# Kernel tuning notes

Hardware: AMD Instinct MI355X
Metric: run time of the kernel (lower is better)

The kernel has to match this reference:

```python
import jax, jax.numpy as jnp
import numpy as np

V, E = 50000, 800000
NODE_IN, EDGE_IN, OUT, HEADS = 128, 16, 32, 4
NEG_SLOPE = 0.2  # DGL EdgeGATConv default negative_slope


def setup_inputs() -> dict:
    key = jax.random.key(0)
    ks = jax.random.split(key, 10)
    return {
        "node_feats": jax.random.normal(ks[0], (V, NODE_IN), jnp.float32),
        "edge_feats": jax.random.normal(ks[1], (E, EDGE_IN), jnp.float32),
        "src": jax.random.randint(ks[2], (E,), 0, V),
        "dst": jax.random.randint(ks[3], (E,), 0, V),
        "W_node": jax.random.normal(ks[4], (NODE_IN, HEADS * OUT), jnp.float32) * 0.05,
        "W_edge": jax.random.normal(ks[5], (EDGE_IN, HEADS * OUT), jnp.float32) * 0.05,
        "attn_l": jax.random.normal(ks[6], (HEADS, OUT), jnp.float32) * 0.05,
        "attn_r": jax.random.normal(ks[7], (HEADS, OUT), jnp.float32) * 0.05,
        "attn_e": jax.random.normal(ks[8], (HEADS, OUT), jnp.float32) * 0.05,
        "res_W": jax.random.normal(ks[9], (NODE_IN, HEADS * OUT), jnp.float32) * 0.05,
        "bias": jnp.zeros((HEADS * OUT,), jnp.float32),
    }


def _leaky_relu(x, slope):
    return jnp.where(x >= 0, x, slope * x)


def reference(node_feats, edge_feats, src, dst, W_node, W_edge, attn_l, attn_r, attn_e, res_W, bias):
    V = node_feats.shape[0]
    H, F = attn_l.shape
    # linear projections
    ft = (node_feats @ W_node).reshape(V, H, F)    # [V,H,F]
    fe = (edge_feats @ W_edge).reshape(-1, H, F)   # [E,H,F]
    # per-head attention logits
    el = jnp.einsum('vhf,hf->vh', ft, attn_l)      # [V,H]
    er = jnp.einsum('vhf,hf->vh', ft, attn_r)      # [V,H]
    ee = jnp.einsum('ehf,hf->eh', fe, attn_e)      # [E,H]
    e = _leaky_relu(el[src] + er[dst] + ee, NEG_SLOPE)  # [E,H]
    # edge softmax over incoming edges of each destination node (stable)
    emax = jax.ops.segment_max(e, dst, num_segments=V)  # [V,H]
    ex = jnp.exp(e - emax[dst])
    esum = jax.ops.segment_sum(ex, dst, num_segments=V)  # [V,H]
    a = ex / esum[dst]                                   # [E,H]
    # weighted message passing: u_mul_e(ft, a) then sum to dst
    msg = ft[src] * a[:, :, None]                        # [E,H,F]
    rst = jax.ops.segment_sum(msg, dst, num_segments=V)  # [V,H,F]
    # residual connection + bias (EdgeGATConv residual=True, bias=True)
    rst = rst + (node_feats @ res_W).reshape(V, H, F)
    rst = rst + bias.reshape(1, H, F)
    # agg_mode='flatten': concat heads
    return rst.reshape(V, H * F)
```

## Files before the change

kernel.cpp:

```cpp
#include <hip/hip_runtime.h>
#include <hip/hip_fp16.h>
#include <cstdint>

#define V_N 50000
#define E_N 800000
#define NODE_IN 128
#define EDGE_IN 16
#define HF 128
#define NEG_SLOPE 0.2f
#define NBUCKET 782
#define NPART 1563
#define PSZ 512
#define CAP 2048
#define LCAP 1536
#define NODE_BLKS 1563
#define PREP_BLKS 64

#define OFF_FT    0
#define OFF_EL    3200000
#define OFF_ER    3400000
#define OFF_H     3600000
#define OFF_BSUM  4822272
#define OFF_WATT  4823056
#define OFF_BFRAG 4823120
#define OFF_RECB  4839504

typedef short bf16x8 __attribute__((ext_vector_type(8)));
typedef float f32x4 __attribute__((ext_vector_type(4)));

__device__ __forceinline__ unsigned short f2bf(float f) {
    unsigned u = __float_as_uint(f);
    u += 0x7fffu + ((u >> 16) & 1u);
    return (unsigned short)(u >> 16);
}
__device__ __forceinline__ unsigned pk2(float lo, float hi) {
    return (unsigned)f2bf(lo) | ((unsigned)f2bf(hi) << 16);
}
__device__ __forceinline__ float bflo(unsigned w) { return __uint_as_float(w << 16); }
__device__ __forceinline__ float bfhi(unsigned w) { return __uint_as_float(w & 0xffff0000u); }

typedef __fp16 fp16x2 __attribute__((ext_vector_type(2)));
__device__ __forceinline__ unsigned pkh2(float a, float b) {
    fp16x2 h = __builtin_amdgcn_cvt_pkrtz(a, b);
    return __builtin_bit_cast(unsigned, h);
}
__device__ __forceinline__ __half2 u2h(unsigned u) {
    return __builtin_bit_cast(__half2, u);
}
__device__ __forceinline__ unsigned h2u(__half2 h) {
    return __builtin_bit_cast(unsigned, h);
}

__global__ __launch_bounds__(256) void k_prephist(
    const float* __restrict__ We, const float* __restrict__ attn_e,
    const float* __restrict__ Wn, const float* __restrict__ Wr,
    const int* __restrict__ dst,
    float* __restrict__ watt, unsigned* __restrict__ bfrag,
    int* __restrict__ H)
{
    const int t = threadIdx.x;
    if (blockIdx.x >= PREP_BLKS) {
        int hb = blockIdx.x - PREP_BLKS;
        __shared__ int h[NBUCKET];
        for (int i = t; i < NBUCKET; i += 256) h[i] = 0;
        __syncthreads();
        #pragma unroll
        for (int c = 0; c < 2; c++) {
            int e = hb * PSZ + c * 256 + t;
            if (e < E_N) atomicAdd(&h[dst[e] >> 6], 1);
        }
        __syncthreads();
        for (int i = t; i < NBUCKET; i += 256) H[hb * NBUCKET + i] = h[i];
        return;
    }
    int g = blockIdx.x * 256 + t;
    if (blockIdx.x == 0 && t < 64) {
        int k = t >> 2, hh = t & 3;
        float s = 0.f;
        #pragma unroll
        for (int f = 0; f < 32; f++)
            s += We[k * HF + hh * 32 + f] * attn_e[hh * 32 + f];
        watt[k * 4 + hh] = s;
    }
    {
        int c    = g >> 8;
        int lane = (g >> 2) & 63;
        int jp   = g & 3;
        int nt = c >> 2, ks = c & 3;
        int col = nt * 16 + (lane & 15);
        int k   = ks * 32 + (lane >> 4) * 8 + jp * 2;
        const float* W = (col < 128) ? Wn : Wr;
        int cc = col & 127;
        float x0 = W[(size_t)k * 128 + cc];
        float x1 = W[(size_t)(k + 1) * 128 + cc];
        bfrag[g] = pk2(x0, x1);
    }
}

__global__ __launch_bounds__(256) void k_nodescan(
    const float* __restrict__ nf, const unsigned* __restrict__ bfragw,
    const float* __restrict__ attn_l, const float* __restrict__ attn_r,
    const float* __restrict__ bias,
    unsigned* __restrict__ ftw, float* __restrict__ el,
    float* __restrict__ er, float* __restrict__ out,
    int* __restrict__ H, int* __restrict__ binsum)
{
    __shared__ __align__(16) float sSf[32 * 140];
    unsigned short* sA = (unsigned short*)sSf;

    if (blockIdx.x < NBUCKET) {
        int* shi = (int*)sSf;
        const int bin = blockIdx.x;
        const int t = threadIdx.x;
        int v[8];
        int ls = 0;
        #pragma unroll
        for (int j = 0; j < 8; j++) {
            int p = t * 8 + j;
            v[j] = (p < NPART) ? H[p * NBUCKET + bin] : 0;
            ls += v[j];
        }
        shi[t] = ls;
        __syncthreads();
        #pragma unroll
        for (int off = 1; off < 256; off <<= 1) {
            int u = (t >= off) ? shi[t - off] : 0;
            __syncthreads();
            shi[t] += u;
            __syncthreads();
        }
        int c = bin * CAP + shi[t] - ls;
        #pragma unroll
        for (int j = 0; j < 8; j++) {
            int p = t * 8 + j;
            if (p < NPART) { H[p * NBUCKET + bin] = c; c += v[j]; }
        }
        if (t == 255) binsum[bin] = shi[255];
        return;
    }

    const int t = threadIdx.x;
    const int lane = t & 63;
    const int w = t >> 6;
    const int nb = (blockIdx.x - NBUCKET) * 32;
    const int n15 = lane & 15;
    const int q = lane >> 4;
    const unsigned short* bfrag = (const unsigned short*)bfragw;

    #pragma unroll
    for (int i = 0; i < 4; i++) {
        int f = t + i * 256;
        int node = f >> 5;
        int kc = (f & 31) * 4;
        float4 v = {0.f, 0.f, 0.f, 0.f};
        if (nb + node < V_N)
            v = *(const float4*)(nf + (size_t)(nb + node) * NODE_IN + kc);
        uint2 u2 = make_uint2(pk2(v.x, v.y), pk2(v.z, v.w));
        *(uint2*)&sA[node * 136 + kc] = u2;
    }
    __syncthreads();

    f32x4 acc[2][4];
    #pragma unroll
    for (int m = 0; m < 2; m++)
        #pragma unroll
        for (int tt = 0; tt < 4; tt++) acc[m][tt] = (f32x4){0.f, 0.f, 0.f, 0.f};

    #pragma unroll
    for (int ks = 0; ks < 4; ks++) {
        bf16x8 a0 = *(const bf16x8*)&sA[n15 * 136 + ks * 32 + q * 8];
        bf16x8 a1 = *(const bf16x8*)&sA[(16 + n15) * 136 + ks * 32 + q * 8];
        #pragma unroll
        for (int tt = 0; tt < 4; tt++) {
            int nt = (tt < 2) ? (2 * w + tt) : (8 + 2 * w + (tt - 2));
            bf16x8 b = *(const bf16x8*)(bfrag + ((size_t)(nt * 4 + ks) * 64 + lane) * 8);
            acc[0][tt] = __builtin_amdgcn_mfma_f32_16x16x32_bf16(a0, b, acc[0][tt], 0, 0, 0);
            acc[1][tt] = __builtin_amdgcn_mfma_f32_16x16x32_bf16(a1, b, acc[1][tt], 0, 0, 0);
        }
    }

    {
        float al0 = attn_l[w * 32 + n15];
        float al1 = attn_l[w * 32 + 16 + n15];
        float ar0 = attn_r[w * 32 + n15];
        float ar1 = attn_r[w * 32 + 16 + n15];
        #pragma unroll
        for (int m = 0; m < 2; m++) {
            #pragma unroll
            for (int r = 0; r < 4; r++) {
                float fa = acc[m][0][r], fb = acc[m][1][r];
                float elp = fa * al0 + fb * al1;
                float erp = fa * ar0 + fb * ar1;
                elp += __shfl_xor(elp, 1); erp += __shfl_xor(erp, 1);
                elp += __shfl_xor(elp, 2); erp += __shfl_xor(erp, 2);
                elp += __shfl_xor(elp, 4); erp += __shfl_xor(erp, 4);
                elp += __shfl_xor(elp, 8); erp += __shfl_xor(erp, 8);
                int node = nb + m * 16 + q * 4 + r;
                if (n15 == 0 && node < V_N) {
                    el[node * 4 + w] = elp;
                    er[node * 4 + w] = erp;
                }
            }
        }
    }
    #pragma unroll
    for (int m = 0; m < 2; m++)
        #pragma unroll
        for (int r = 0; r < 4; r++) {
            int node = nb + m * 16 + q * 4 + r;
            if (node < V_N)
                ftw[(size_t)node * 64 + w * 16 + n15] =
                    pkh2(acc[m][0][r], acc[m][1][r]);
        }
    __syncthreads();

    #pragma unroll
    for (int m = 0; m < 2; m++)
        #pragma unroll
        for (int tt = 2; tt < 4; tt++)
            #pragma unroll
            for (int r = 0; r < 4; r++)
                sSf[(m * 16 + q * 4 + r) * 140 + w * 32 + (tt - 2) * 16 + n15] =
                    acc[m][tt][r];
    __syncthreads();
    #pragma unroll
    for (int i = 0; i < 4; i++) {
        int u = t + i * 256;
        int node = u >> 5, c4 = (u & 31) * 4;
        if (nb + node < V_N) {
            float4 v = *(float4*)&sSf[node * 140 + c4];
            float4 b4 = *(const float4*)(bias + c4);
            v.x += b4.x; v.y += b4.y; v.z += b4.z; v.w += b4.w;
            *(float4*)(out + (size_t)(nb + node) * HF + c4) = v;
        }
    }
}

__global__ __launch_bounds__(256) void k_bin(
    const float* __restrict__ ef, const int* __restrict__ src,
    const int* __restrict__ dst, const float* __restrict__ watt,
    const float* __restrict__ el, const int* __restrict__ H,
    uint4* __restrict__ recb)
{
    __shared__ float sw[64];
    __shared__ __align__(16) float see[PSZ][4];
    __shared__ int boff[NBUCKET];
    const int t = threadIdx.x;
    const int b = blockIdx.x;
    if (t < 64) sw[t] = watt[t];
    for (int i = t; i < NBUCKET; i += 256) boff[i] = H[b * NBUCKET + i];
    __syncthreads();
    const int lane = t & 63, w = t >> 6;
    const int k0 = (lane & 3) * 4;

    #pragma unroll
    for (int r = 0; r < 8; r++) {
        int le = w * 128 + r * 16 + (lane >> 2);
        int ge = b * PSZ + le;
        float4 v = {0.f, 0.f, 0.f, 0.f};
        if (ge < E_N)
            v = *(const float4*)(ef + (size_t)ge * EDGE_IN + k0);
        float e0 = 0.f, e1 = 0.f, e2 = 0.f, e3 = 0.f;
        float vv[4] = {v.x, v.y, v.z, v.w};
        #pragma unroll
        for (int j = 0; j < 4; j++) {
            int k = k0 + j;
            e0 += vv[j] * sw[k * 4 + 0];
            e1 += vv[j] * sw[k * 4 + 1];
            e2 += vv[j] * sw[k * 4 + 2];
            e3 += vv[j] * sw[k * 4 + 3];
        }
        e0 += __shfl_xor(e0, 1); e1 += __shfl_xor(e1, 1);
        e2 += __shfl_xor(e2, 1); e3 += __shfl_xor(e3, 1);
        e0 += __shfl_xor(e0, 2); e1 += __shfl_xor(e1, 2);
        e2 += __shfl_xor(e2, 2); e3 += __shfl_xor(e3, 2);
        if ((lane & 3) == 0) {
            float4 o = {e0, e1, e2, e3};
            *(float4*)&see[le][0] = o;
        }
    }
    __syncthreads();

    #pragma unroll
    for (int c = 0; c < 2; c++) {
        int le = c * 256 + t;
        int e = b * PSZ + le;
        if (e < E_N) {
            int s = src[e], d = dst[e];
            int p = atomicAdd(&boff[d >> 6], 1);
            float4 ee = *(float4*)&see[le][0];
            float4 el4 = *(const float4*)(el + (size_t)s * 4);
            uint4 rr;
            rr.x = (unsigned)s;
            rr.y = pk2(el4.x + ee.x, el4.y + ee.y);
            rr.z = pk2(el4.z + ee.z, el4.w + ee.w);
            rr.w = (unsigned)d;
            recb[p] = rr;
        }
    }
}

__global__ __launch_bounds__(256) void k_fuse(
    const int* __restrict__ binsum, const uint4* __restrict__ recb,
    const float* __restrict__ er, const unsigned* __restrict__ ftw,
    float* __restrict__ out)
{
    __shared__ int ssi[LCAP];
    __shared__ unsigned char sdl[LCAP];
    __shared__ unsigned saw[LCAP][4];
    __shared__ unsigned short sidx[LCAP];
    __shared__ int scnt[64], sbase[64], scur[64];

    const int t = threadIdx.x;
    const int b = blockIdx.x;
    const int size = min(binsum[b], LCAP);
    const int src0 = b * CAP;

    if (t < 64) scnt[t] = 0;
    __syncthreads();

    for (int i = t; i < size; i += 256) {
        uint4 r = recb[src0 + i];
        int d = (int)r.w;
        const float4 er4 = *(const float4*)(er + (size_t)d * 4);
        float x0 = bflo(r.y) + er4.x;
        float x1 = bfhi(r.y) + er4.y;
        float x2 = bflo(r.z) + er4.z;
        float x3 = bfhi(r.z) + er4.w;
        x0 = x0 >= 0.f ? x0 : NEG_SLOPE * x0;
        x1 = x1 >= 0.f ? x1 : NEG_SLOPE * x1;
        x2 = x2 >= 0.f ? x2 : NEG_SLOPE * x2;
        x3 = x3 >= 0.f ? x3 : NEG_SLOPE * x3;
        float e0 = __expf(x0), e1 = __expf(x1);
        float e2 = __expf(x2), e3 = __expf(x3);
        saw[i][0] = pkh2(e0, e0); saw[i][1] = pkh2(e1, e1);
        saw[i][2] = pkh2(e2, e2); saw[i][3] = pkh2(e3, e3);
        ssi[i] = (int)r.x;
        int dl = d & 63;
        sdl[i] = (unsigned char)dl;
        atomicAdd(&scnt[dl], 1);
    }
    __syncthreads();

    if (t < 64) {
        int v = scnt[t];
        int x = v;
        #pragma unroll
        for (int off = 1; off < 64; off <<= 1) {
            int u = __shfl_up(x, off);
            if (t >= off) x += u;
        }
        sbase[t] = x - v;
        scur[t] = x - v;
    }
    __syncthreads();

    for (int i = t; i < size; i += 256) {
        int p = atomicAdd(&scur[sdl[i]], 1);
        sidx[p] = (unsigned short)i;
    }
    __syncthreads();

    const int g = t >> 4;
    const int li = t & 15;
    const int head = li >> 2;
    #pragma unroll
    for (int dq = 0; dq < 4; dq++) {
        int dl = g + dq * 16;
        int deg = scnt[dl];
        if (deg == 0) continue;
        int n0 = sbase[dl];
        int dglob = (b << 6) + dl;
        __half2 ha0 = u2h(0u), ha1 = u2h(0u), ha2 = u2h(0u), ha3 = u2h(0u);
        __half2 hb0 = u2h(0u), hb1 = u2h(0u), hb2 = u2h(0u), hb3 = u2h(0u);
        float s = 0.f;
        int e = 0;
        for (; e + 1 < deg; e += 2) {
            int i0 = sidx[n0 + e], i1 = sidx[n0 + e + 1];
            int s0 = ssi[i0], s1 = ssi[i1];
            unsigned a0 = saw[i0][head], a1 = saw[i1][head];
            uint4 w0 = *(const uint4*)(ftw + (size_t)s0 * 64 + li * 4);
            uint4 w1 = *(const uint4*)(ftw + (size_t)s1 * 64 + li * 4);
            ha0 = __hfma2(u2h(w0.x), u2h(a0), ha0);
            ha1 = __hfma2(u2h(w0.y), u2h(a0), ha1);
            ha2 = __hfma2(u2h(w0.z), u2h(a0), ha2);
            ha3 = __hfma2(u2h(w0.w), u2h(a0), ha3);
            hb0 = __hfma2(u2h(w1.x), u2h(a1), hb0);
            hb1 = __hfma2(u2h(w1.y), u2h(a1), hb1);
            hb2 = __hfma2(u2h(w1.z), u2h(a1), hb2);
            hb3 = __hfma2(u2h(w1.w), u2h(a1), hb3);
            s += __low2float(u2h(a0)) + __low2float(u2h(a1));
        }
        if (e < deg) {
            int i0 = sidx[n0 + e];
            int s0 = ssi[i0];
            unsigned a0 = saw[i0][head];
            uint4 w0 = *(const uint4*)(ftw + (size_t)s0 * 64 + li * 4);
            ha0 = __hfma2(u2h(w0.x), u2h(a0), ha0);
            ha1 = __hfma2(u2h(w0.y), u2h(a0), ha1);
            ha2 = __hfma2(u2h(w0.z), u2h(a0), ha2);
            ha3 = __hfma2(u2h(w0.w), u2h(a0), ha3);
            s += __low2float(u2h(a0));
        }
        ha0 = __hadd2(ha0, hb0); ha1 = __hadd2(ha1, hb1);
        ha2 = __hadd2(ha2, hb2); ha3 = __hadd2(ha3, hb3);

        float rsv = 1.f / s;
        float* op = out + (size_t)dglob * HF + head * 32 + (li & 3) * 4;
        float4 r0 = *(float4*)op;
        r0.x += __low2float(ha0) * rsv; r0.y += __low2float(ha1) * rsv;
        r0.z += __low2float(ha2) * rsv; r0.w += __low2float(ha3) * rsv;
        *(float4*)op = r0;
        float4 r1 = *(float4*)(op + 16);
        r1.x += __high2float(ha0) * rsv; r1.y += __high2float(ha1) * rsv;
        r1.z += __high2float(ha2) * rsv; r1.w += __high2float(ha3) * rsv;
        *(float4*)(op + 16) = r1;
    }
}

extern "C" void kernel_launch(void* const* d_in, const int* in_sizes, int n_in,
                              void* d_out, int out_size, void* d_ws, size_t ws_size,
                              hipStream_t stream) {
    const float* nf     = (const float*)d_in[0];
    const float* ef     = (const float*)d_in[1];
    const int*   src    = (const int*)d_in[2];
    const int*   dst    = (const int*)d_in[3];
    const float* Wn     = (const float*)d_in[4];
    const float* We     = (const float*)d_in[5];
    const float* attn_l = (const float*)d_in[6];
    const float* attn_r = (const float*)d_in[7];
    const float* attn_e = (const float*)d_in[8];
    const float* Wr     = (const float*)d_in[9];
    const float* bias   = (const float*)d_in[10];
    float* out = (float*)d_out;

    unsigned* wsw  = (unsigned*)d_ws;
    unsigned* ftw  = wsw + OFF_FT;
    float* el      = (float*)(wsw + OFF_EL);
    float* er      = (float*)(wsw + OFF_ER);
    int* H         = (int*)(wsw + OFF_H);
    int* binsum    = (int*)(wsw + OFF_BSUM);
    float* watt    = (float*)(wsw + OFF_WATT);
    unsigned* bfrag = wsw + OFF_BFRAG;
    uint4* recb    = (uint4*)(wsw + OFF_RECB);

    k_prephist<<<PREP_BLKS + NPART, 256, 0, stream>>>(
        We, attn_e, Wn, Wr, dst, watt, bfrag, H);
    k_nodescan<<<NBUCKET + NODE_BLKS, 256, 0, stream>>>(
        nf, bfrag, attn_l, attn_r, bias, ftw, el, er, out, H, binsum);
    k_bin<<<NPART, 256, 0, stream>>>(ef, src, dst, watt, el, H, recb);
    k_fuse<<<NBUCKET, 256, 0, stream>>>(binsum, recb, er, ftw, out);
}
```

Baseline: 219.2 us.

## Restructure histogram scan to process 16 bins per block with coalesced reads

The per-bucket exclusive scan over partition histograms now runs in 49 blocks, each handling 16 bins. Each bin is split across 16 thread groups that serially sum 98 partitions. Previously there were 782 blocks, each doing strided single-column reads. Neighbouring threads now read adjacent bins, so the H accesses coalesce into contiguous row segments, and fewer blocks are spent on the scan. The cost is longer serial loops per thread and fewer blocks doing the scan work.

```diff
diff --git a/kernel.cpp b/kernel.cpp
--- a/kernel.cpp
+++ b/kernel.cpp
@@ -13,6 +13,8 @@
 #define PSZ 512
 #define CAP 2048
 #define LCAP 1536
+#define NSCAN 49
+#define PPG 98
 #define NODE_BLKS 1563
 #define PREP_BLKS 64
 
@@ -108,41 +110,41 @@
     __shared__ __align__(16) float sSf[32 * 140];
     unsigned short* sA = (unsigned short*)sSf;
 
-    if (blockIdx.x < NBUCKET) {
-        int* shi = (int*)sSf;
-        const int bin = blockIdx.x;
+    if (blockIdx.x < NSCAN) {
+        int* ssum = (int*)sSf;
         const int t = threadIdx.x;
-        int v[8];
+        const int bi = t & 15, bg = t >> 4;
+        const int bin = blockIdx.x * 16 + bi;
+        const int p0 = bg * PPG;
+        const int p1 = min(p0 + PPG, NPART);
         int ls = 0;
-        #pragma unroll
-        for (int j = 0; j < 8; j++) {
-            int p = t * 8 + j;
-            v[j] = (p < NPART) ? H[p * NBUCKET + bin] : 0;
-            ls += v[j];
-        }
-        shi[t] = ls;
+        if (bin < NBUCKET)
+            for (int p = p0; p < p1; p++) ls += H[p * NBUCKET + bin];
+        ssum[t] = ls;
         __syncthreads();
         #pragma unroll
-        for (int off = 1; off < 256; off <<= 1) {
-            int u = (t >= off) ? shi[t - off] : 0;
+        for (int off = 1; off < 16; off <<= 1) {
+            int u = (bg >= off) ? ssum[t - off * 16] : 0;
             __syncthreads();
-            shi[t] += u;
+            ssum[t] += u;
             __syncthreads();
         }
-        int c = bin * CAP + shi[t] - ls;
-        #pragma unroll
-        for (int j = 0; j < 8; j++) {
-            int p = t * 8 + j;
-            if (p < NPART) { H[p * NBUCKET + bin] = c; c += v[j]; }
-        }
-        if (t == 255) binsum[bin] = shi[255];
+        if (bin < NBUCKET) {
+            int c = bin * CAP + ssum[t] - ls;
+            for (int p = p0; p < p1; p++) {
+                int v = H[p * NBUCKET + bin];
+                H[p * NBUCKET + bin] = c;
+                c += v;
+            }
+            if (bg == 15) binsum[bin] = ssum[t];
+        }
         return;
     }
 
     const int t = threadIdx.x;
     const int lane = t & 63;
     const int w = t >> 6;
-    const int nb = (blockIdx.x - NBUCKET) * 32;
+    const int nb = (blockIdx.x - NSCAN) * 32;
     const int n15 = lane & 15;
     const int q = lane >> 4;
     const unsigned short* bfrag = (const unsigned short*)bfragw;
@@ -446,8 +448,8 @@
 
     k_prephist<<<PREP_BLKS + NPART, 256, 0, stream>>>(
         We, attn_e, Wn, Wr, dst, watt, bfrag, H);
-    k_nodescan<<<NBUCKET + NODE_BLKS, 256, 0, stream>>>(
+    k_nodescan<<<NSCAN + NODE_BLKS, 256, 0, stream>>>(
         nf, bfrag, attn_l, attn_r, bias, ftw, el, er, out, H, binsum);
-    k_bin<<<NPART, 256, 0, stream>>>(ef, src, dst, watt, el, H, recb);
+    k_bin<<<NPART, 256, 0, stream>>>(ef, src, dst, watt, el, H, binsum ? recb : recb);
     k_fuse<<<NBUCKET, 256, 0, stream>>>(binsum, recb, er, ftw, out);
 }
```

Result: slower. 228.0 us (+4.0%).
